# Performance work log

Hardware: AMD Instinct MI355X
Metric: run time of the kernel (lower is better)

The kernel has to match this reference:

```python
import jax, jax.numpy as jnp
import numpy as np

HEADS = 8
DIM_HEAD = 64
DOWN = 2

def setup_inputs() -> dict:
    key = jax.random.key(0)
    ks = jax.random.split(key, 6)
    shp = (1, 128, 16, 32, 32)
    inner = HEADS * DIM_HEAD  # 512
    return {
        "x": jax.random.normal(ks[0], shp, dtype=jnp.float32),
        "context": jax.random.normal(ks[1], shp, dtype=jnp.float32),
        "Wq": jax.random.normal(ks[2], (inner, 128), dtype=jnp.float32) * 0.02,
        "Wk": jax.random.normal(ks[3], (inner, 128), dtype=jnp.float32) * 0.02,
        "Wv": jax.random.normal(ks[4], (inner, 128), dtype=jnp.float32) * 0.02,
        "Wo": jax.random.normal(ks[5], (128, inner), dtype=jnp.float32) * 0.02,
    }

def _avg_pool3d(c, f):
    b, ch, d, h, w = c.shape
    return c.reshape(b, ch, d // f, f, h // f, f, w // f, f).mean(axis=(3, 5, 7))

def reference(x, context, Wq, Wk, Wv, Wo):
    b, c, d1, h1, w1 = x.shape
    n = d1 * h1 * w1
    scale = DIM_HEAD ** -0.5
    xf = x.reshape(b, c, n)  # [b, c, N]
    # 1x1x1 conv == channel matmul
    q = jnp.einsum('oc,bcn->bon', Wq, xf).reshape(b, HEADS, DIM_HEAD, n)
    q = jnp.swapaxes(q, -2, -1)  # [b, h, N, dh]
    ctx = _avg_pool3d(context, DOWN)
    _, _, d2, h2, w2 = ctx.shape
    m = d2 * h2 * w2
    cf = ctx.reshape(b, c, m)
    k = jnp.einsum('oc,bcm->bom', Wk, cf).reshape(b, HEADS, DIM_HEAD, m)  # [b,h,dh,M]
    v = jnp.einsum('oc,bcm->bom', Wv, cf).reshape(b, HEADS, DIM_HEAD, m)
    v = jnp.swapaxes(v, -2, -1)  # [b, h, M, dh]
    scores = jnp.einsum('bhnd,bhdm->bhnm', q, k) * scale  # [b,h,N,M]
    attn = jax.nn.softmax(scores, axis=-1)
    out = jnp.einsum('bhnm,bhmd->bhnd', attn, v)  # [b,h,N,dh]
    out = jnp.swapaxes(out, -2, -1).reshape(b, HEADS * DIM_HEAD, n)  # [b,inner,N]
    y = jnp.einsum('oc,bcn->bon', Wo, out)
    return y.reshape(b, -1, d1, h1, w1)
```

## Files before the change

kernel.cpp:

```cpp
#include <hip/hip_runtime.h>

#define N_TOK 16384
#define M_TOK 2048
#define NHEADS 8
#define DH 64
#define CIN 128
#define INNER 512

typedef __attribute__((ext_vector_type(8))) short bf16x8;
typedef __attribute__((ext_vector_type(16))) float f32x16;
typedef __attribute__((ext_vector_type(4))) unsigned int u32x4;
typedef __attribute__((ext_vector_type(2))) unsigned int u32x2;

#if __has_builtin(__builtin_amdgcn_exp2f)
#define QS 0.18033688011112042f
#define EXPF(x) __builtin_amdgcn_exp2f(x)
#else
#define QS 0.125f
#define EXPF(x) __expf(x)
#endif

__device__ __forceinline__ unsigned short f2bf(float f) {
    unsigned u = __float_as_uint(f);
    u += 0x7fff + ((u >> 16) & 1);
    return (unsigned short)(u >> 16);
}

__device__ __forceinline__ unsigned cvtpk(float lo, float hi) {
    unsigned r;
    asm("v_cvt_pk_bf16_f32 %0, %1, %2" : "=v"(r) : "v"(lo), "v"(hi));
    return r;
}

__device__ __forceinline__ bf16x8 mk_bf16x8(unsigned a, unsigned b, unsigned c, unsigned d) {
    union { u32x4 w; bf16x8 h; } u;
    u.w = (u32x4){a, b, c, d};
    return u.h;
}

__device__ __forceinline__ void gload16(const void* g, void* l) {
    __builtin_amdgcn_global_load_lds(
        (const __attribute__((address_space(1))) unsigned int*)g,
        (__attribute__((address_space(3))) unsigned int*)l, 16, 0, 0);
}

__global__ __launch_bounds__(256) void prep_k(const float* __restrict__ Wq,
                                              const float* __restrict__ Wo,
                                              const float* __restrict__ cin,
                                              const float* __restrict__ x,
                                              unsigned short* __restrict__ Wqb,
                                              unsigned short* __restrict__ Wob,
                                              float* __restrict__ cout,
                                              unsigned short* __restrict__ xb) {
    __shared__ unsigned short tile[64 * 132];
    const int t = threadIdx.x;
    if (blockIdx.x < 64) {
        int i = (blockIdx.x * 256 + t) * 8;
        const float* src; unsigned short* dst; float sc;
        if (i < 65536) { src = Wq + i; dst = Wqb + i; sc = QS; }
        else           { src = Wo + (i - 65536); dst = Wob + (i - 65536); sc = 1.0f; }
        float4 a = *reinterpret_cast<const float4*>(src);
        float4 b = *reinterpret_cast<const float4*>(src + 4);
        unsigned short u[8] = { f2bf(a.x * sc), f2bf(a.y * sc), f2bf(a.z * sc), f2bf(a.w * sc),
                                f2bf(b.x * sc), f2bf(b.y * sc), f2bf(b.z * sc), f2bf(b.w * sc) };
        *reinterpret_cast<uint4*>(dst) = *reinterpret_cast<uint4*>(u);
    } else if (blockIdx.x < 1088) {
        int idx = (blockIdx.x - 64) * 256 + t;
        int c = idx >> 11, m = idx & 2047;
        int d2 = m >> 8, h2 = (m >> 4) & 15, w2 = m & 15;
        const float* b = cin + c * 16384 + d2 * 2048 + h2 * 64 + w2 * 2;
        float s = b[0] + b[1] + b[32] + b[33] + b[1024] + b[1025] + b[1056] + b[1057];
        cout[idx] = s * 0.125f;
    } else {
        const int xbid = blockIdx.x - 1088;
        const int n0 = (xbid & 127) * 128;
        const int cb = (xbid >> 7) * 64;
#pragma unroll
        for (int cc2 = 0; cc2 < 2; ++cc2)
#pragma unroll
            for (int lp = 0; lp < 4; ++lp) {
                int id = lp * 256 + t;
                int row = id >> 5, ch = id & 31;
                float4 v = *reinterpret_cast<const float4*>(
                    &x[(size_t)(cb + cc2 * 32 + row) * N_TOK + n0 + ch * 4]);
                unsigned short u[4] = { f2bf(v.x), f2bf(v.y), f2bf(v.z), f2bf(v.w) };
                *reinterpret_cast<uint2*>(&tile[(cc2 * 32 + row) * 132 + ch * 4]) =
                    *reinterpret_cast<uint2*>(u);
            }
        __syncthreads();
#pragma unroll
        for (int lp = 0; lp < 4; ++lp) {
            int id = lp * 256 + t;
            int n = id >> 3, cg = id & 7;
            unsigned short u[8];
#pragma unroll
            for (int j = 0; j < 8; ++j) u[j] = tile[(cg * 8 + j) * 132 + n];
            *reinterpret_cast<uint4*>(&xb[(size_t)(n0 + n) * 128 + cb + cg * 8]) =
                *reinterpret_cast<uint4*>(u);
        }
    }
}

__global__ __launch_bounds__(256) void projs_k(const float* __restrict__ ctx,
                                               const float* __restrict__ Wk,
                                               const float* __restrict__ Wv,
                                               const unsigned short* __restrict__ Wqb,
                                               const unsigned short* __restrict__ xb,
                                               unsigned short* __restrict__ Kb,
                                               unsigned short* __restrict__ Vb,
                                               unsigned short* __restrict__ Qb) {
    const int b = blockIdx.x;
    const int t = threadIdx.x;
    if (b < 1024) {
        const int bx = b & 3, by = (b >> 2) & 127, bz = b >> 9;
        const int m0 = (bx * 256 + t) * 2;
        const int o0 = by * 4;
        const float* W = bz ? Wv : Wk;
        float acc[4][2];
#pragma unroll
        for (int j = 0; j < 4; ++j) { acc[j][0] = 0.f; acc[j][1] = 0.f; }
        for (int c4 = 0; c4 < CIN / 4; ++c4) {
            float xa[4][2];
#pragma unroll
            for (int cc = 0; cc < 4; ++cc)
                *reinterpret_cast<float2*>(xa[cc]) =
                    *reinterpret_cast<const float2*>(&ctx[(size_t)(c4 * 4 + cc) * M_TOK + m0]);
#pragma unroll
            for (int j = 0; j < 4; ++j) {
                float4 wv = *reinterpret_cast<const float4*>(&W[(o0 + j) * CIN + c4 * 4]);
#pragma unroll
                for (int k = 0; k < 2; ++k) {
                    acc[j][k] = fmaf(wv.x, xa[0][k], acc[j][k]);
                    acc[j][k] = fmaf(wv.y, xa[1][k], acc[j][k]);
                    acc[j][k] = fmaf(wv.z, xa[2][k], acc[j][k]);
                    acc[j][k] = fmaf(wv.w, xa[3][k], acc[j][k]);
                }
            }
        }
        if (bz) {
#pragma unroll
            for (int j = 0; j < 4; ++j) {
                unsigned w0 = (unsigned)f2bf(acc[j][0]) | ((unsigned)f2bf(acc[j][1]) << 16);
                *reinterpret_cast<unsigned*>(&Vb[(size_t)(o0 + j) * M_TOK + m0]) = w0;
            }
        } else {
            const int h = o0 >> 6, d0 = o0 & 63;
#pragma unroll
            for (int k = 0; k < 2; ++k) {
                unsigned short u[4];
#pragma unroll
                for (int j = 0; j < 4; ++j) u[j] = f2bf(acc[j][k]);
                *reinterpret_cast<uint2*>(&Kb[((size_t)h * M_TOK + m0 + k) * DH + d0]) =
                    *reinterpret_cast<uint2*>(u);
            }
        }
    } else {
        const int bid = b - 1024;
        const int w = t >> 6, l = t & 63;
        const int la = l & 31, lg = l >> 5;
        const int n = bid * 32 + la;

        bf16x8 bx[8];
#pragma unroll
        for (int ks = 0; ks < 8; ++ks)
            bx[ks] = *reinterpret_cast<const bf16x8*>(xb + (size_t)n * 128 + ks * 16 + lg * 8);

        f32x16 acc[4];
#pragma unroll
        for (int os = 0; os < 4; ++os) acc[os] = (f32x16){0,0,0,0,0,0,0,0,0,0,0,0,0,0,0,0};

#pragma unroll
        for (int os = 0; os < 4; ++os) {
            const int row = w * 128 + os * 32 + la;
#pragma unroll
            for (int ks = 0; ks < 8; ++ks) {
                bf16x8 aw = *reinterpret_cast<const bf16x8*>(Wqb + (size_t)row * 128 + ks * 16 + lg * 8);
                acc[os] = __builtin_amdgcn_mfma_f32_32x32x16_bf16(aw, bx[ks], acc[os], 0, 0, 0);
            }
        }
#pragma unroll
        for (int os = 0; os < 4; ++os) {
            const int h = w * 2 + (os >> 1);
            const int dbase = (os & 1) * 32 + 4 * lg;
#pragma unroll
            for (int rr = 0; rr < 4; ++rr) {
                unsigned p0 = cvtpk(acc[os][rr * 4 + 0], acc[os][rr * 4 + 1]);
                unsigned p1 = cvtpk(acc[os][rr * 4 + 2], acc[os][rr * 4 + 3]);
                uint2 pv = make_uint2(p0, p1);
                *reinterpret_cast<uint2*>(&Qb[((size_t)h * N_TOK + n) * DH + dbase + rr * 8]) = pv;
            }
        }
    }
}

__global__ __launch_bounds__(512, 4) void attn_k(const unsigned short* __restrict__ Qb,
                                                 const unsigned short* __restrict__ Kb,
                                                 const unsigned short* __restrict__ Vb,
                                                 unsigned short* __restrict__ Ob) {
    __shared__ __align__(16) char smem[65536];

    const int t = threadIdx.x;
    const int w = t >> 6, l = t & 63;
    const int la = l & 31, lg = l >> 5;
    const int bid = blockIdx.x;
    const int h = bid & 7;
    const int n0 = (bid >> 3) * 256;

    bf16x8 aq[4];
    {
        const unsigned short* qrow = Qb + ((size_t)h * N_TOK + n0 + w * 32 + la) * DH + lg * 8;
#pragma unroll
        for (int ks = 0; ks < 4; ++ks)
            aq[ks] = *reinterpret_cast<const bf16x8*>(qrow + ks * 16);
    }

    const bf16x8 vone = mk_bf16x8(0x3F803F80u, 0x3F803F80u, 0x3F803F80u, 0x3F803F80u);

    const char* gK = (const char*)Kb + (size_t)h * M_TOK * 128;
    const char* gV = (const char*)Vb + (size_t)h * DH * 4096;

    auto stage = [&](int b, int tile) {
        char* buf = smem + b * 32768;
#pragma unroll
        for (int i = 0; i < 2; ++i) {
            int c = t + i * 512;
            int row = c >> 3, o16 = (c & 7) << 4;
            gload16(gK + (size_t)(tile * 128 + row) * 128 + (o16 ^ ((row & 7) << 4)),
                    buf + c * 16);
            int vrow = c >> 4, vo16 = (c & 15) << 4;
            gload16(gV + (size_t)vrow * 4096 + tile * 256 + (vo16 ^ ((vrow & 7) << 4)),
                    buf + 16384 + c * 16);
        }
    };

    f32x16 oacc0 = {0,0,0,0,0,0,0,0,0,0,0,0,0,0,0,0};
    f32x16 oacc1 = {0,0,0,0,0,0,0,0,0,0,0,0,0,0,0,0};
    f32x16 oaccS = {0,0,0,0,0,0,0,0,0,0,0,0,0,0,0,0};

    stage(0, 0);
    __syncthreads();

#pragma unroll 2
    for (int mt = 0; mt < M_TOK / 128; ++mt) {
        const int cb = (mt & 1) * 32768;
        if (mt < M_TOK / 128 - 1) stage((mt & 1) ^ 1, mt + 1);

#pragma unroll
        for (int ms = 0; ms < 4; ++ms) {
            f32x16 sacc = {0,0,0,0,0,0,0,0,0,0,0,0,0,0,0,0};
            __builtin_amdgcn_s_setprio(1);
#pragma unroll
            for (int ks = 0; ks < 4; ++ks) {
                const int row = ms * 32 + la;
                bf16x8 ak = *reinterpret_cast<const bf16x8*>(
                    smem + cb + row * 128 + ((32 * ks + 16 * lg) ^ ((row & 7) << 4)));
                sacc = __builtin_amdgcn_mfma_f32_32x32x16_bf16(ak, aq[ks], sacc, 0, 0, 0);
            }
            __builtin_amdgcn_s_setprio(0);
            float p[16];
#pragma unroll
            for (int r = 0; r < 16; ++r) p[r] = EXPF(sacc[r]);
            u32x2 s0 = __builtin_amdgcn_permlane32_swap(cvtpk(p[0], p[1]),  cvtpk(p[4], p[5]),  false, false);
            u32x2 s1 = __builtin_amdgcn_permlane32_swap(cvtpk(p[2], p[3]),  cvtpk(p[6], p[7]),  false, false);
            u32x2 s2 = __builtin_amdgcn_permlane32_swap(cvtpk(p[8], p[9]),  cvtpk(p[12], p[13]), false, false);
            u32x2 s3 = __builtin_amdgcn_permlane32_swap(cvtpk(p[10], p[11]), cvtpk(p[14], p[15]), false, false);
            bf16x8 pa0 = mk_bf16x8(s0.x, s1.x, s0.y, s1.y);
            bf16x8 pa1 = mk_bf16x8(s2.x, s3.x, s2.y, s3.y);
            __builtin_amdgcn_s_setprio(1);
            oaccS = __builtin_amdgcn_mfma_f32_32x32x16_bf16(pa0, vone, oaccS, 0, 0, 0);
            oaccS = __builtin_amdgcn_mfma_f32_32x32x16_bf16(pa1, vone, oaccS, 0, 0, 0);
            {
                const int vrow = la, vs = (vrow & 7) << 4;
                const char* vb = smem + cb + 16384 + vrow * 256;
                bf16x8 bv0 = *reinterpret_cast<const bf16x8*>(vb + ((64 * ms + 16 * lg) ^ vs));
                bf16x8 bv1 = *reinterpret_cast<const bf16x8*>(vb + ((64 * ms + 32 + 16 * lg) ^ vs));
                oacc0 = __builtin_amdgcn_mfma_f32_32x32x16_bf16(pa0, bv0, oacc0, 0, 0, 0);
                oacc0 = __builtin_amdgcn_mfma_f32_32x32x16_bf16(pa1, bv1, oacc0, 0, 0, 0);
            }
            {
                const int vrow = 32 + la, vs = (vrow & 7) << 4;
                const char* vb = smem + cb + 16384 + vrow * 256;
                bf16x8 bv0 = *reinterpret_cast<const bf16x8*>(vb + ((64 * ms + 16 * lg) ^ vs));
                bf16x8 bv1 = *reinterpret_cast<const bf16x8*>(vb + ((64 * ms + 32 + 16 * lg) ^ vs));
                oacc1 = __builtin_amdgcn_mfma_f32_32x32x16_bf16(pa0, bv0, oacc1, 0, 0, 0);
                oacc1 = __builtin_amdgcn_mfma_f32_32x32x16_bf16(pa1, bv1, oacc1, 0, 0, 0);
            }
            __builtin_amdgcn_s_setprio(0);
        }
        __syncthreads();
    }

    float inv[16];
#pragma unroll
    for (int r = 0; r < 16; ++r) inv[r] = __builtin_amdgcn_rcpf(oaccS[r]);

    float* Ot = reinterpret_cast<float*>(smem);
#pragma unroll
    for (int pass = 0; pass < 2; ++pass) {
        __syncthreads();
        if ((w >> 2) == pass) {
            const int wl = w & 3;
#pragma unroll
            for (int dt = 0; dt < 2; ++dt)
#pragma unroll
                for (int r = 0; r < 16; r += 2) {
                    int d = dt * 32 + la;
                    int n = wl * 32 + (r & 3) + 8 * (r >> 2) + 4 * lg;
                    float2 v;
                    v.x = (dt ? oacc1[r] : oacc0[r]) * inv[r];
                    v.y = (dt ? oacc1[r + 1] : oacc0[r + 1]) * inv[r + 1];
                    *reinterpret_cast<float2*>(&Ot[d * 132 + n]) = v;
                }
        }
        __syncthreads();
#pragma unroll
        for (int i = 0; i < 2; ++i) {
            int id = i * 512 + t;
            int n = id & 127, dg = id >> 7;
            unsigned q[4];
#pragma unroll
            for (int jj = 0; jj < 4; ++jj)
                q[jj] = cvtpk(Ot[(dg * 8 + jj * 2) * 132 + n],
                              Ot[(dg * 8 + jj * 2 + 1) * 132 + n]);
            *reinterpret_cast<uint4*>(&Ob[(size_t)(n0 + pass * 128 + n) * INNER + h * 64 + dg * 8]) =
                *reinterpret_cast<uint4*>(q);
        }
    }
}

__global__ __launch_bounds__(256) void yproj_k(const unsigned short* __restrict__ Wob,
                                               const unsigned short* __restrict__ Ob,
                                               float* __restrict__ y) {
    const int t = threadIdx.x;
    const int w = t >> 6, l = t & 63;
    const int la = l & 31, lg = l >> 5;
    const int n = blockIdx.x * 32 + la;
    const int row = w * 32 + la;

    f32x16 acc = {0,0,0,0,0,0,0,0,0,0,0,0,0,0,0,0};
#pragma unroll 8
    for (int ks = 0; ks < 32; ++ks) {
        bf16x8 bo = *reinterpret_cast<const bf16x8*>(Ob + (size_t)n * INNER + ks * 16 + lg * 8);
        bf16x8 aw = *reinterpret_cast<const bf16x8*>(Wob + (size_t)row * INNER + ks * 16 + lg * 8);
        acc = __builtin_amdgcn_mfma_f32_32x32x16_bf16(aw, bo, acc, 0, 0, 0);
    }
#pragma unroll
    for (int rr = 0; rr < 4; ++rr)
#pragma unroll
        for (int q = 0; q < 4; ++q) {
            int o = w * 32 + 4 * lg + rr * 8 + q;
            y[(size_t)o * N_TOK + n] = acc[rr * 4 + q];
        }
}

extern "C" void kernel_launch(void* const* d_in, const int* in_sizes, int n_in,
                              void* d_out, int out_size, void* d_ws, size_t ws_size,
                              hipStream_t stream) {
    const float* x   = (const float*)d_in[0];
    const float* ctx = (const float*)d_in[1];
    const float* Wq  = (const float*)d_in[2];
    const float* Wk  = (const float*)d_in[3];
    const float* Wv  = (const float*)d_in[4];
    const float* Wo  = (const float*)d_in[5];
    float* y = (float*)d_out;

    char* W = (char*)d_ws;
    float* ctxp         = (float*)(W);
    unsigned short* Kb  = (unsigned short*)(W + 1u  * (1 << 20));
    unsigned short* Vb  = (unsigned short*)(W + 3u  * (1 << 20));
    unsigned short* xb  = (unsigned short*)(W + 5u  * (1 << 20));
    unsigned short* Wqb = (unsigned short*)(W + 9u  * (1 << 20));
    unsigned short* Wob = (unsigned short*)(W + 9u  * (1 << 20) + (256 << 10));
    unsigned short* Qb  = (unsigned short*)(W + 10u * (1 << 20));
    unsigned short* Ob  = (unsigned short*)(W + 26u * (1 << 20));

    prep_k<<<dim3(64 + 1024 + 256), 256, 0, stream>>>(Wq, Wo, ctx, x, Wqb, Wob, ctxp, xb);
    projs_k<<<dim3(1024 + N_TOK / 32), 256, 0, stream>>>(ctxp, Wk, Wv, Wqb, xb, Kb, Vb, Qb);
    attn_k<<<dim3(N_TOK / 256 * NHEADS), 512, 0, stream>>>(Qb, Kb, Vb, Ob);
    yproj_k<<<dim3(N_TOK / 32), 256, 0, stream>>>(Wob, Ob, y);
}
```

Measured before the change: 130.7 us.

## Halve attention block and KV tile sizes, split fused projection kernel in two

The attention kernel now uses 256 threads covering 128 queries per block instead of 512 threads and 256 queries, and stages 64-key K/V tiles into double-buffered shared memory of about 34 KB. The V tile layout and swizzle are adjusted for 128-byte rows, and the output epilogue becomes a single pass. This aims at more resident blocks per CU and better latency hiding. In exchange each K/V tile is reused by fewer queries and the kernel runs twice as many loop iterations and barriers. The fused K/V/Q projection kernel is also split back into two separate launches, which adds launch overhead and removes overlap between the two projections.

New measurement: 139.0 us. 1.06x slower.

```diff
diff --git a/kernel.cpp b/kernel.cpp
--- a/kernel.cpp
+++ b/kernel.cpp
@@ -101,110 +101,106 @@
     }
 }
 
-__global__ __launch_bounds__(256) void projs_k(const float* __restrict__ ctx,
-                                               const float* __restrict__ Wk,
-                                               const float* __restrict__ Wv,
-                                               const unsigned short* __restrict__ Wqb,
+__global__ __launch_bounds__(256) void kvproj_k(const float* __restrict__ ctx,
+                                                const float* __restrict__ Wk,
+                                                const float* __restrict__ Wv,
+                                                unsigned short* __restrict__ Kb,
+                                                unsigned short* __restrict__ Vb) {
+    const int m0 = (blockIdx.x * 256 + threadIdx.x) * 2;
+    const int o0 = blockIdx.y * 4;
+    const float* W = blockIdx.z ? Wv : Wk;
+    float acc[4][2];
+#pragma unroll
+    for (int j = 0; j < 4; ++j) { acc[j][0] = 0.f; acc[j][1] = 0.f; }
+    for (int c4 = 0; c4 < CIN / 4; ++c4) {
+        float xa[4][2];
+#pragma unroll
+        for (int cc = 0; cc < 4; ++cc)
+            *reinterpret_cast<float2*>(xa[cc]) =
+                *reinterpret_cast<const float2*>(&ctx[(size_t)(c4 * 4 + cc) * M_TOK + m0]);
+#pragma unroll
+        for (int j = 0; j < 4; ++j) {
+            float4 wv = *reinterpret_cast<const float4*>(&W[(o0 + j) * CIN + c4 * 4]);
+#pragma unroll
+            for (int k = 0; k < 2; ++k) {
+                acc[j][k] = fmaf(wv.x, xa[0][k], acc[j][k]);
+                acc[j][k] = fmaf(wv.y, xa[1][k], acc[j][k]);
+                acc[j][k] = fmaf(wv.z, xa[2][k], acc[j][k]);
+                acc[j][k] = fmaf(wv.w, xa[3][k], acc[j][k]);
+            }
+        }
+    }
+    if (blockIdx.z) {
+#pragma unroll
+        for (int j = 0; j < 4; ++j) {
+            unsigned w0 = (unsigned)f2bf(acc[j][0]) | ((unsigned)f2bf(acc[j][1]) << 16);
+            *reinterpret_cast<unsigned*>(&Vb[(size_t)(o0 + j) * M_TOK + m0]) = w0;
+        }
+    } else {
+        const int h = o0 >> 6, d0 = o0 & 63;
+#pragma unroll
+        for (int k = 0; k < 2; ++k) {
+            unsigned short u[4];
+#pragma unroll
+            for (int j = 0; j < 4; ++j) u[j] = f2bf(acc[j][k]);
+            *reinterpret_cast<uint2*>(&Kb[((size_t)h * M_TOK + m0 + k) * DH + d0]) =
+                *reinterpret_cast<uint2*>(u);
+        }
+    }
+}
+
+__global__ __launch_bounds__(256) void qproj_k(const unsigned short* __restrict__ Wqb,
                                                const unsigned short* __restrict__ xb,
-                                               unsigned short* __restrict__ Kb,
-                                               unsigned short* __restrict__ Vb,
                                                unsigned short* __restrict__ Qb) {
-    const int b = blockIdx.x;
     const int t = threadIdx.x;
-    if (b < 1024) {
-        const int bx = b & 3, by = (b >> 2) & 127, bz = b >> 9;
-        const int m0 = (bx * 256 + t) * 2;
-        const int o0 = by * 4;
-        const float* W = bz ? Wv : Wk;
-        float acc[4][2];
-#pragma unroll
-        for (int j = 0; j < 4; ++j) { acc[j][0] = 0.f; acc[j][1] = 0.f; }
-        for (int c4 = 0; c4 < CIN / 4; ++c4) {
-            float xa[4][2];
-#pragma unroll
-            for (int cc = 0; cc < 4; ++cc)
-                *reinterpret_cast<float2*>(xa[cc]) =
-                    *reinterpret_cast<const float2*>(&ctx[(size_t)(c4 * 4 + cc) * M_TOK + m0]);
-#pragma unroll
-            for (int j = 0; j < 4; ++j) {
-                float4 wv = *reinterpret_cast<const float4*>(&W[(o0 + j) * CIN + c4 * 4]);
-#pragma unroll
-                for (int k = 0; k < 2; ++k) {
-                    acc[j][k] = fmaf(wv.x, xa[0][k], acc[j][k]);
-                    acc[j][k] = fmaf(wv.y, xa[1][k], acc[j][k]);
-                    acc[j][k] = fmaf(wv.z, xa[2][k], acc[j][k]);
-                    acc[j][k] = fmaf(wv.w, xa[3][k], acc[j][k]);
-                }
-            }
-        }
-        if (bz) {
-#pragma unroll
-            for (int j = 0; j < 4; ++j) {
-                unsigned w0 = (unsigned)f2bf(acc[j][0]) | ((unsigned)f2bf(acc[j][1]) << 16);
-                *reinterpret_cast<unsigned*>(&Vb[(size_t)(o0 + j) * M_TOK + m0]) = w0;
-            }
-        } else {
-            const int h = o0 >> 6, d0 = o0 & 63;
-#pragma unroll
-            for (int k = 0; k < 2; ++k) {
-                unsigned short u[4];
-#pragma unroll
-                for (int j = 0; j < 4; ++j) u[j] = f2bf(acc[j][k]);
-                *reinterpret_cast<uint2*>(&Kb[((size_t)h * M_TOK + m0 + k) * DH + d0]) =
-                    *reinterpret_cast<uint2*>(u);
-            }
-        }
-    } else {
-        const int bid = b - 1024;
-        const int w = t >> 6, l = t & 63;
-        const int la = l & 31, lg = l >> 5;
-        const int n = bid * 32 + la;
-
-        bf16x8 bx[8];
-#pragma unroll
-        for (int ks = 0; ks < 8; ++ks)
-            bx[ks] = *reinterpret_cast<const bf16x8*>(xb + (size_t)n * 128 + ks * 16 + lg * 8);
-
-        f32x16 acc[4];
-#pragma unroll
-        for (int os = 0; os < 4; ++os) acc[os] = (f32x16){0,0,0,0,0,0,0,0,0,0,0,0,0,0,0,0};
-
-#pragma unroll
-        for (int os = 0; os < 4; ++os) {
-            const int row = w * 128 + os * 32 + la;
-#pragma unroll
-            for (int ks = 0; ks < 8; ++ks) {
-                bf16x8 aw = *reinterpret_cast<const bf16x8*>(Wqb + (size_t)row * 128 + ks * 16 + lg * 8);
-                acc[os] = __builtin_amdgcn_mfma_f32_32x32x16_bf16(aw, bx[ks], acc[os], 0, 0, 0);
-            }
-        }
-#pragma unroll
-        for (int os = 0; os < 4; ++os) {
-            const int h = w * 2 + (os >> 1);
-            const int dbase = (os & 1) * 32 + 4 * lg;
-#pragma unroll
-            for (int rr = 0; rr < 4; ++rr) {
-                unsigned p0 = cvtpk(acc[os][rr * 4 + 0], acc[os][rr * 4 + 1]);
-                unsigned p1 = cvtpk(acc[os][rr * 4 + 2], acc[os][rr * 4 + 3]);
-                uint2 pv = make_uint2(p0, p1);
-                *reinterpret_cast<uint2*>(&Qb[((size_t)h * N_TOK + n) * DH + dbase + rr * 8]) = pv;
-            }
-        }
-    }
-}
-
-__global__ __launch_bounds__(512, 4) void attn_k(const unsigned short* __restrict__ Qb,
+    const int w = t >> 6, l = t & 63;
+    const int la = l & 31, lg = l >> 5;
+    const int n = blockIdx.x * 32 + la;
+
+    bf16x8 bx[8];
+#pragma unroll
+    for (int ks = 0; ks < 8; ++ks)
+        bx[ks] = *reinterpret_cast<const bf16x8*>(xb + (size_t)n * 128 + ks * 16 + lg * 8);
+
+    f32x16 acc[4];
+#pragma unroll
+    for (int os = 0; os < 4; ++os) acc[os] = (f32x16){0,0,0,0,0,0,0,0,0,0,0,0,0,0,0,0};
+
+#pragma unroll
+    for (int os = 0; os < 4; ++os) {
+        const int row = w * 128 + os * 32 + la;
+#pragma unroll
+        for (int ks = 0; ks < 8; ++ks) {
+            bf16x8 aw = *reinterpret_cast<const bf16x8*>(Wqb + (size_t)row * 128 + ks * 16 + lg * 8);
+            acc[os] = __builtin_amdgcn_mfma_f32_32x32x16_bf16(aw, bx[ks], acc[os], 0, 0, 0);
+        }
+    }
+#pragma unroll
+    for (int os = 0; os < 4; ++os) {
+        const int h = w * 2 + (os >> 1);
+        const int dbase = (os & 1) * 32 + 4 * lg;
+#pragma unroll
+        for (int rr = 0; rr < 4; ++rr) {
+            unsigned p0 = cvtpk(acc[os][rr * 4 + 0], acc[os][rr * 4 + 1]);
+            unsigned p1 = cvtpk(acc[os][rr * 4 + 2], acc[os][rr * 4 + 3]);
+            uint2 pv = make_uint2(p0, p1);
+            *reinterpret_cast<uint2*>(&Qb[((size_t)h * N_TOK + n) * DH + dbase + rr * 8]) = pv;
+        }
+    }
+}
+
+__global__ __launch_bounds__(256, 4) void attn_k(const unsigned short* __restrict__ Qb,
                                                  const unsigned short* __restrict__ Kb,
                                                  const unsigned short* __restrict__ Vb,
                                                  unsigned short* __restrict__ Ob) {
-    __shared__ __align__(16) char smem[65536];
+    __shared__ __align__(16) char smem[34816];
 
     const int t = threadIdx.x;
     const int w = t >> 6, l = t & 63;
     const int la = l & 31, lg = l >> 5;
     const int bid = blockIdx.x;
     const int h = bid & 7;
-    const int n0 = (bid >> 3) * 256;
+    const int n0 = (bid >> 3) * 128;
 
     bf16x8 aq[4];
     {
@@ -220,16 +216,15 @@
     const char* gV = (const char*)Vb + (size_t)h * DH * 4096;
 
     auto stage = [&](int b, int tile) {
-        char* buf = smem + b * 32768;
+        char* buf = smem + b * 16384;
 #pragma unroll
         for (int i = 0; i < 2; ++i) {
-            int c = t + i * 512;
+            int c = t + i * 256;
             int row = c >> 3, o16 = (c & 7) << 4;
-            gload16(gK + (size_t)(tile * 128 + row) * 128 + (o16 ^ ((row & 7) << 4)),
+            gload16(gK + (size_t)(tile * 64 + row) * 128 + (o16 ^ ((row & 7) << 4)),
                     buf + c * 16);
-            int vrow = c >> 4, vo16 = (c & 15) << 4;
-            gload16(gV + (size_t)vrow * 4096 + tile * 256 + (vo16 ^ ((vrow & 7) << 4)),
-                    buf + 16384 + c * 16);
+            gload16(gV + (size_t)row * 4096 + tile * 128 + (o16 ^ ((row & 7) << 4)),
+                    buf + 8192 + c * 16);
         }
     };
 
@@ -241,12 +236,12 @@
     __syncthreads();
 
 #pragma unroll 2
-    for (int mt = 0; mt < M_TOK / 128; ++mt) {
-        const int cb = (mt & 1) * 32768;
-        if (mt < M_TOK / 128 - 1) stage((mt & 1) ^ 1, mt + 1);
-
-#pragma unroll
-        for (int ms = 0; ms < 4; ++ms) {
+    for (int mt = 0; mt < M_TOK / 64; ++mt) {
+        const int cb = (mt & 1) * 16384;
+        if (mt < M_TOK / 64 - 1) stage((mt & 1) ^ 1, mt + 1);
+
+#pragma unroll
+        for (int ms = 0; ms < 2; ++ms) {
             f32x16 sacc = {0,0,0,0,0,0,0,0,0,0,0,0,0,0,0,0};
             __builtin_amdgcn_s_setprio(1);
 #pragma unroll
@@ -271,7 +266,7 @@
             oaccS = __builtin_amdgcn_mfma_f32_32x32x16_bf16(pa1, vone, oaccS, 0, 0, 0);
             {
                 const int vrow = la, vs = (vrow & 7) << 4;
-                const char* vb = smem + cb + 16384 + vrow * 256;
+                const char* vb = smem + cb + 8192 + vrow * 128;
                 bf16x8 bv0 = *reinterpret_cast<const bf16x8*>(vb + ((64 * ms + 16 * lg) ^ vs));
                 bf16x8 bv1 = *reinterpret_cast<const bf16x8*>(vb + ((64 * ms + 32 + 16 * lg) ^ vs));
                 oacc0 = __builtin_amdgcn_mfma_f32_32x32x16_bf16(pa0, bv0, oacc0, 0, 0, 0);
@@ -279,7 +274,7 @@
             }
             {
                 const int vrow = 32 + la, vs = (vrow & 7) << 4;
-                const char* vb = smem + cb + 16384 + vrow * 256;
+                const char* vb = smem + cb + 8192 + vrow * 128;
                 bf16x8 bv0 = *reinterpret_cast<const bf16x8*>(vb + ((64 * ms + 16 * lg) ^ vs));
                 bf16x8 bv1 = *reinterpret_cast<const bf16x8*>(vb + ((64 * ms + 32 + 16 * lg) ^ vs));
                 oacc1 = __builtin_amdgcn_mfma_f32_32x32x16_bf16(pa0, bv0, oacc1, 0, 0, 0);
@@ -296,35 +291,28 @@
 
     float* Ot = reinterpret_cast<float*>(smem);
 #pragma unroll
-    for (int pass = 0; pass < 2; ++pass) {
-        __syncthreads();
-        if ((w >> 2) == pass) {
-            const int wl = w & 3;
-#pragma unroll
-            for (int dt = 0; dt < 2; ++dt)
-#pragma unroll
-                for (int r = 0; r < 16; r += 2) {
-                    int d = dt * 32 + la;
-                    int n = wl * 32 + (r & 3) + 8 * (r >> 2) + 4 * lg;
-                    float2 v;
-                    v.x = (dt ? oacc1[r] : oacc0[r]) * inv[r];
-                    v.y = (dt ? oacc1[r + 1] : oacc0[r + 1]) * inv[r + 1];
-                    *reinterpret_cast<float2*>(&Ot[d * 132 + n]) = v;
-                }
-        }
-        __syncthreads();
-#pragma unroll
-        for (int i = 0; i < 2; ++i) {
-            int id = i * 512 + t;
-            int n = id & 127, dg = id >> 7;
-            unsigned q[4];
-#pragma unroll
-            for (int jj = 0; jj < 4; ++jj)
-                q[jj] = cvtpk(Ot[(dg * 8 + jj * 2) * 132 + n],
-                              Ot[(dg * 8 + jj * 2 + 1) * 132 + n]);
-            *reinterpret_cast<uint4*>(&Ob[(size_t)(n0 + pass * 128 + n) * INNER + h * 64 + dg * 8]) =
-                *reinterpret_cast<uint4*>(q);
-        }
+    for (int dt = 0; dt < 2; ++dt)
+#pragma unroll
+        for (int r = 0; r < 16; r += 2) {
+            int d = dt * 32 + la;
+            int n = w * 32 + (r & 3) + 8 * (r >> 2) + 4 * lg;
+            float2 v;
+            v.x = (dt ? oacc1[r] : oacc0[r]) * inv[r];
+            v.y = (dt ? oacc1[r + 1] : oacc0[r + 1]) * inv[r + 1];
+            *reinterpret_cast<float2*>(&Ot[d * 132 + n]) = v;
+        }
+    __syncthreads();
+#pragma unroll
+    for (int i = 0; i < 4; ++i) {
+        int id = i * 256 + t;
+        int n = id & 127, dg = id >> 7;
+        unsigned q[4];
+#pragma unroll
+        for (int jj = 0; jj < 4; ++jj)
+            q[jj] = cvtpk(Ot[(dg * 8 + jj * 2) * 132 + n],
+                          Ot[(dg * 8 + jj * 2 + 1) * 132 + n]);
+        *reinterpret_cast<uint4*>(&Ob[(size_t)(n0 + n) * INNER + h * 64 + dg * 8]) =
+            *reinterpret_cast<uint4*>(q);
     }
 }
 
@@ -375,7 +363,8 @@
     unsigned short* Ob  = (unsigned short*)(W + 26u * (1 << 20));
 
     prep_k<<<dim3(64 + 1024 + 256), 256, 0, stream>>>(Wq, Wo, ctx, x, Wqb, Wob, ctxp, xb);
-    projs_k<<<dim3(1024 + N_TOK / 32), 256, 0, stream>>>(ctxp, Wk, Wv, Wqb, xb, Kb, Vb, Qb);
-    attn_k<<<dim3(N_TOK / 256 * NHEADS), 512, 0, stream>>>(Qb, Kb, Vb, Ob);
+    kvproj_k<<<dim3(M_TOK / 512, INNER / 4, 2), 256, 0, stream>>>(ctxp, Wk, Wv, Kb, Vb);
+    qproj_k<<<dim3(N_TOK / 32), 256, 0, stream>>>(Wqb, xb, Qb);
+    attn_k<<<dim3(N_TOK / 128 * NHEADS), 256, 0, stream>>>(Qb, Kb, Vb, Ob);
     yproj_k<<<dim3(N_TOK / 32), 256, 0, stream>>>(Wob, Ob, y);
 }
```
